# Optimization experiments

Hardware: AMD Instinct MI355X
Metric: run time of the kernel (lower is better)

## Reference

```python
import jax, jax.numpy as jnp
import numpy as np

B, R, T, D = 16, 1024, 512, 1024
H = 1024  # hidden_dim

def setup_inputs() -> dict:
    key = jax.random.key(0)
    ks = jax.random.split(key, 8)
    s_in = 1.0 / np.sqrt(D)
    s_comb = 1.0 / np.sqrt(3 * D)
    return {
        "region_feats": jax.random.normal(ks[0], (B, R, D), jnp.float32),
        "query_embs": jax.random.normal(ks[1], (B, T, D), jnp.float32),
        "Wr": jax.random.normal(ks[2], (D, H), jnp.float32) * s_in,
        "br": jnp.zeros((H,), jnp.float32),
        "Wq": jax.random.normal(ks[3], (D, H), jnp.float32) * s_in,
        "bq": jnp.zeros((H,), jnp.float32),
        "Ws": jax.random.normal(ks[4], (3 * D, 1), jnp.float32) * s_comb,
        "bs": jnp.zeros((1,), jnp.float32),
    }

def reference(region_feats, query_embs, Wr, br, Wq, bq, Ws, bs):
    # Dense projections
    R_proj = region_feats @ Wr + br            # [B,R,H]
    Q_proj = query_embs @ Wq + bq              # [B,T,H]
    # Unscaled cross-attention scores
    scores = jnp.einsum('brd,btd->brt', R_proj, Q_proj)  # [B,R,T]
    attn = jax.nn.softmax(scores, axis=-1)
    # Attend over RAW query embeddings (as in source)
    attended = jnp.einsum('brt,btd->brd', attn, query_embs)  # [B,R,D]
    combined = jnp.concatenate(
        [region_feats, attended, region_feats * attended], axis=-1)  # [B,R,3D]
    out = combined @ Ws + bs                    # [B,R,1]
    return jnp.squeeze(out, axis=-1)            # [B,R]
```

## Files before the change

### kernel.cpp

```cpp
#include <hip/hip_runtime.h>


#define BD 16
#define RD 1024
#define TD 512
#define DD 1024
#define BR (BD * RD)

typedef _Float16 half8 __attribute__((ext_vector_type(8)));
typedef _Float16 half4 __attribute__((ext_vector_type(4)));
typedef float floatx4 __attribute__((ext_vector_type(4)));

__device__ __forceinline__ float wave_sum(float v) {
#pragma unroll
  for (int off = 32; off > 0; off >>= 1) v += __shfl_down(v, off);
  return v;
}

__device__ __forceinline__ half8 cvt8(float4 a, float4 b) {
  half8 h = {(_Float16)a.x, (_Float16)a.y, (_Float16)a.z, (_Float16)a.w,
             (_Float16)b.x, (_Float16)b.y, (_Float16)b.z, (_Float16)b.w};
  return h;
}

__global__ __launch_bounds__(256) void prep_all(
    const float* __restrict__ Wr, const float* __restrict__ Wq,
    const float* __restrict__ Ws, const float* __restrict__ br,
    const float* __restrict__ region, const float* __restrict__ query,
    _Float16* __restrict__ M2, _Float16* __restrict__ Ws16,
    float* __restrict__ wqbr, _Float16* __restrict__ wqbr16,
    _Float16* __restrict__ r16, float* __restrict__ rdvec,
    _Float16* __restrict__ q16) {
  __shared__ __align__(16) _Float16 lds[2 * 2 * 2048];
  __shared__ float sm[4];
  const int blk = blockIdx.x, tid = threadIdx.x;

  if (blk < 256) {
    const int m0 = (blk >> 4) * 64, n0 = (blk & 15) * 64;
    const int lane = tid & 63, w = tid >> 6;
    const int wr = w >> 1, wc = w & 1;
    const int srow = tid >> 2, slot = tid & 3;
    const int scol = (slot ^ ((srow >> 1) & 3)) * 8;
    const long offA = (long)(m0 + srow) * DD + scol;
    const long offB = (long)(n0 + srow) * DD + scol;
    const int wofs = srow * 32 + slot * 8;
    const int NK = DD / 32;
    float4 a0, a1, b0, b1;
    a0 = *(const float4*)(Wr + offA); a1 = *(const float4*)(Wr + offA + 4);
    b0 = *(const float4*)(Wq + offB); b1 = *(const float4*)(Wq + offB + 4);
    *(int4*)&lds[wofs] = *(int4*)&(const half8&)cvt8(a0, a1);
    {
      half8 hb = cvt8(b0, b1);
      *(half8*)&lds[2048 + wofs] = hb;
    }
    a0 = *(const float4*)(Wr + offA + 32); a1 = *(const float4*)(Wr + offA + 36);
    b0 = *(const float4*)(Wq + offB + 32); b1 = *(const float4*)(Wq + offB + 36);
    __syncthreads();
    floatx4 acc[2][2] = {};
    const int fr = lane & 15, g = lane >> 4;
    const int fs = (g ^ ((fr >> 1) & 3)) * 8;
    for (int kt = 0; kt < NK; ++kt) {
      const int cur = (kt & 1) * 4096, nxt = ((kt + 1) & 1) * 4096;
      if (kt + 1 < NK) {
        half8 ha = cvt8(a0, a1), hb = cvt8(b0, b1);
        *(half8*)&lds[nxt + wofs] = ha;
        *(half8*)&lds[nxt + 2048 + wofs] = hb;
      }
      if (kt + 2 < NK) {
        const long go = (long)(kt + 2) * 32;
        a0 = *(const float4*)(Wr + offA + go); a1 = *(const float4*)(Wr + offA + go + 4);
        b0 = *(const float4*)(Wq + offB + go); b1 = *(const float4*)(Wq + offB + go + 4);
      }
      half8 af[2], bf[2];
#pragma unroll
      for (int i = 0; i < 2; ++i)
        af[i] = *(const half8*)&lds[cur + (32 * wr + 16 * i + fr) * 32 + fs];
#pragma unroll
      for (int j = 0; j < 2; ++j)
        bf[j] = *(const half8*)&lds[cur + 2048 + (32 * wc + 16 * j + fr) * 32 + fs];
#pragma unroll
      for (int i = 0; i < 2; ++i)
#pragma unroll
        for (int j = 0; j < 2; ++j)
          acc[i][j] = __builtin_amdgcn_mfma_f32_16x16x32_f16(af[i], bf[j], acc[i][j], 0, 0, 0);
      __syncthreads();
    }
    const int cr = g * 4, cc = fr;
#pragma unroll
    for (int i = 0; i < 2; ++i)
#pragma unroll
      for (int r = 0; r < 4; ++r)
#pragma unroll
        for (int j = 0; j < 2; ++j)
          M2[(long)(m0 + 32 * wr + 16 * i + cr + r) * DD + n0 + 32 * wc + 16 * j + cc] =
              (_Float16)acc[i][j][r];
  } else if (blk < 258) {
    const long i = (long)(blk - 256) * 1024 + tid * 4;
    const float4 v = *(const float4*)&Ws[DD + i];
    half4 h = {(_Float16)v.x, (_Float16)v.y, (_Float16)v.z, (_Float16)v.w};
    *(half4*)&Ws16[i] = h;
  } else if (blk < 514) {
    const int row = (blk - 258) * 4 + (tid >> 6);
    const int lane = tid & 63;
    const float* x = Wq + (long)row * DD;
    float s = 0.f;
    for (int k = lane; k < DD; k += 64) s += x[k] * br[k];
    s = wave_sum(s);
    if (lane == 0) {
      wqbr[row] = s;
      wqbr16[row] = (_Float16)s;
    }
  } else if (blk < 514 + BR) {
    const long row = blk - 514;
    const int lane = tid & 63, wid = tid >> 6;
    const long i = row * DD + tid * 4;
    const float4 v = *(const float4*)&region[i];
    half4 h = {(_Float16)v.x, (_Float16)v.y, (_Float16)v.z, (_Float16)v.w};
    *(half4*)&r16[i] = h;
    const float4 w0 = *(const float4*)&Ws[tid * 4];
    float rd = v.x * w0.x + v.y * w0.y + v.z * w0.z + v.w * w0.w;
    rd = wave_sum(rd);
    if (lane == 0) sm[wid] = rd;
    __syncthreads();
    if (tid == 0) rdvec[row] = sm[0] + sm[1] + sm[2] + sm[3];
  } else {
    const long row = blk - (514 + BR);
    const long i = row * DD + tid * 4;
    const float4 v = *(const float4*)&query[i];
    half4 h = {(_Float16)v.x, (_Float16)v.y, (_Float16)v.z, (_Float16)v.w};
    *(half4*)&q16[i] = h;
  }
}

__global__ __launch_bounds__(512, 4) void qp_gemm(
    const _Float16* __restrict__ A, const _Float16* __restrict__ B,
    _Float16* __restrict__ C, const _Float16* __restrict__ wq16,
    float* __restrict__ cvec) {
  __shared__ __align__(16) _Float16 lds[2 * 2 * 4096];
  const int lin = blockIdx.x;
  const int s = lin & 7, u = lin >> 3;
  const int mt = s * 8 + (u >> 3), nt = u & 7;
  const int m0 = mt * 128, n0 = nt * 128;
  const int tid = threadIdx.x, lane = tid & 63, w = tid >> 6;
  const int wr = w >> 1, wc = w & 1;

  const int lrow = lane >> 2, slot = lane & 3;
  const int scol = (slot ^ ((lrow >> 1) & 3)) * 8;
  const int srow = 16 * w + lrow;
  const _Float16* gA = A + (long)(m0 + srow) * DD + scol;
  const _Float16* gB = B + (long)(n0 + srow) * DD + scol;
  const int wofs = srow * 32 + slot * 8;

  const int NK = DD / 32;
  float cvp = 0.f;
  int4 pA, pB;
  pA = *(const int4*)gA;
  pB = *(const int4*)gB;
  {
    half8 qa, wb;
    __builtin_memcpy(&qa, &pA, 16);
    wb = *(const half8*)&wq16[scol];
#pragma unroll
    for (int e = 0; e < 8; ++e) cvp += (float)qa[e] * (float)wb[e];
  }
  *(int4*)&lds[wofs] = pA;
  *(int4*)&lds[4096 + wofs] = pB;
  pA = *(const int4*)(gA + 32);
  pB = *(const int4*)(gB + 32);
  __syncthreads();

  floatx4 acc[2][4] = {};
  const int fr = lane & 15, g = lane >> 4;
  const int fs = (g ^ ((fr >> 1) & 3)) * 8;

  for (int kt = 0; kt < NK; ++kt) {
    const int cur = (kt & 1) * 8192, nxt = ((kt + 1) & 1) * 8192;
    if (kt + 1 < NK) {
      half8 qa, wb;
      __builtin_memcpy(&qa, &pA, 16);
      wb = *(const half8*)&wq16[(kt + 1) * 32 + scol];
#pragma unroll
      for (int e = 0; e < 8; ++e) cvp += (float)qa[e] * (float)wb[e];
      *(int4*)&lds[nxt + wofs] = pA;
      *(int4*)&lds[nxt + 4096 + wofs] = pB;
    }
    if (kt + 2 < NK) {
      const long go = (long)(kt + 2) * 32;
      pA = *(const int4*)(gA + go);
      pB = *(const int4*)(gB + go);
    }
    half8 af[2], bf[4];
#pragma unroll
    for (int i = 0; i < 2; ++i)
      af[i] = *(const half8*)&lds[cur + (32 * wr + 16 * i + fr) * 32 + fs];
#pragma unroll
    for (int j = 0; j < 4; ++j)
      bf[j] = *(const half8*)&lds[cur + 4096 + (64 * wc + 16 * j + fr) * 32 + fs];
#pragma unroll
    for (int i = 0; i < 2; ++i)
#pragma unroll
      for (int j = 0; j < 4; ++j)
        acc[i][j] = __builtin_amdgcn_mfma_f32_16x16x32_f16(af[i], bf[j], acc[i][j], 0, 0, 0);
    __syncthreads();
  }

  cvp += __shfl_xor(cvp, 1);
  cvp += __shfl_xor(cvp, 2);
  if (nt == 0 && slot == 0) cvec[m0 + srow] = cvp;

  const int cr = g * 4, cc = fr;
#pragma unroll
  for (int i = 0; i < 2; ++i)
#pragma unroll
    for (int r = 0; r < 4; ++r)
#pragma unroll
      for (int j = 0; j < 4; ++j)
        C[(long)(m0 + 32 * wr + 16 * i + cr + r) * DD + n0 + 64 * wc + 16 * j + cc] =
            (_Float16)acc[i][j][r];
}

__global__ __launch_bounds__(512, 4) void gemm_fused(
    const _Float16* __restrict__ A, const _Float16* __restrict__ B0,
    const _Float16* __restrict__ B1,
    float* __restrict__ Ms, float* __restrict__ Ls, float* __restrict__ Hs,
    const float* __restrict__ cvec, const _Float16* __restrict__ wsh,
    long sA, long sB) {
  __shared__ __align__(16) _Float16 lds[2 * 3 * 4096];
  __shared__ __align__(16) _Float16 wlds[2048];

  const int lin = blockIdx.x;
  const int s = lin & 7, u = lin >> 3;
  const int b = 2 * s + (u >> 5);
  const int t = u & 31;
  const int mt = t >> 2, nt = t & 3;
  const int m0 = mt * 128, n0 = nt * 128;
  A += (long)b * sA;
  B0 += (long)b * sB;
  B1 += (long)b * sB;

  const int tid = threadIdx.x, lane = tid & 63, w = tid >> 6;
  const int wr = w >> 2, wc = w & 3;

  const int lrow = lane >> 2, slot = lane & 3;
  const int scol = (slot ^ ((lrow >> 1) & 3)) * 8;
  const int srow = 16 * w + lrow;
  const _Float16* gA = A + (long)(m0 + srow) * DD + scol;
  const _Float16* gP = B0 + (long)(n0 + srow) * DD + scol;
  const _Float16* gQ = B1 + (long)(n0 + srow) * DD + scol;
  const int wofs = srow * 32 + slot * 8;

  if (tid < 256) *(int4*)&wlds[tid * 8] = *(const int4*)&wsh[tid * 8];

  const int NK = DD / 32;
  int4 pA, pP, pQ;
  pA = *(const int4*)gA;
  pP = *(const int4*)gP;
  pQ = *(const int4*)gQ;
  *(int4*)&lds[wofs] = pA;
  *(int4*)&lds[4096 + wofs] = pP;
  *(int4*)&lds[8192 + wofs] = pQ;
  pA = *(const int4*)(gA + 32);
  pP = *(const int4*)(gP + 32);
  pQ = *(const int4*)(gQ + 32);
  __syncthreads();

  floatx4 accS[4][2] = {};
  floatx4 accH[4][2] = {};
  const int fr = lane & 15, g = lane >> 4;
  const int fs = (g ^ ((fr >> 1) & 3)) * 8;

  for (int kt = 0; kt < NK; ++kt) {
    const int cur = (kt & 1) * 12288;
    const int nxt = ((kt + 1) & 1) * 12288;
    if (kt + 1 < NK) {
      *(int4*)&lds[nxt + wofs] = pA;
      *(int4*)&lds[nxt + 4096 + wofs] = pP;
      *(int4*)&lds[nxt + 8192 + wofs] = pQ;
    }
    if (kt + 2 < NK) {
      const long go = (long)(kt + 2) * 32;
      pA = *(const int4*)(gA + go);
      pP = *(const int4*)(gP + go);
      pQ = *(const int4*)(gQ + go);
    }
    half8 af[4], bp[2], bq[2], w1f, w2f;
#pragma unroll
    for (int i = 0; i < 4; ++i)
      af[i] = *(const half8*)&lds[cur + (64 * wr + 16 * i + fr) * 32 + fs];
#pragma unroll
    for (int j = 0; j < 2; ++j)
      bp[j] = *(const half8*)&lds[cur + 4096 + (32 * wc + 16 * j + fr) * 32 + fs];
#pragma unroll
    for (int j = 0; j < 2; ++j)
      bq[j] = *(const half8*)&lds[cur + 8192 + (32 * wc + 16 * j + fr) * 32 + fs];
    w1f = *(const half8*)&wlds[kt * 32 + g * 8];
    w2f = *(const half8*)&wlds[1024 + kt * 32 + g * 8];
#pragma unroll
    for (int i = 0; i < 4; ++i)
#pragma unroll
      for (int j = 0; j < 2; ++j)
        accS[i][j] = __builtin_amdgcn_mfma_f32_16x16x32_f16(af[i], bp[j], accS[i][j], 0, 0, 0);
#pragma unroll
    for (int i = 0; i < 4; ++i) af[i] = w1f + af[i] * w2f;
#pragma unroll
    for (int i = 0; i < 4; ++i)
#pragma unroll
      for (int j = 0; j < 2; ++j)
        accH[i][j] = __builtin_amdgcn_mfma_f32_16x16x32_f16(af[i], bq[j], accH[i][j], 0, 0, 0);
    __syncthreads();
  }

  const int cr = g * 4, cc = fr;
  float cv[2];
#pragma unroll
  for (int j = 0; j < 2; ++j)
    cv[j] = cvec[(long)b * TD + n0 + 32 * wc + 16 * j + cc];
  const int chunk = nt * 4 + wc;
  const long rowBase = (long)b * RD + m0 + 64 * wr + cr;
#pragma unroll
  for (int i = 0; i < 4; ++i) {
#pragma unroll
    for (int r = 0; r < 4; ++r) {
      float mx = fmaxf(accS[i][0][r] + cv[0], accS[i][1][r] + cv[1]);
      mx = fmaxf(mx, __shfl_xor(mx, 1));
      mx = fmaxf(mx, __shfl_xor(mx, 2));
      mx = fmaxf(mx, __shfl_xor(mx, 4));
      mx = fmaxf(mx, __shfl_xor(mx, 8));
      float l = 0.f, hs = 0.f;
#pragma unroll
      for (int j = 0; j < 2; ++j) {
        const float e = __expf(accS[i][j][r] + cv[j] - mx);
        l += e;
        hs += e * accH[i][j][r];
      }
      l += __shfl_xor(l, 1); hs += __shfl_xor(hs, 1);
      l += __shfl_xor(l, 2); hs += __shfl_xor(hs, 2);
      l += __shfl_xor(l, 4); hs += __shfl_xor(hs, 4);
      l += __shfl_xor(l, 8); hs += __shfl_xor(hs, 8);
      if (cc == 0) {
        const long idx = (long)chunk * BR + rowBase + 16 * i + r;
        Ms[idx] = mx;
        Ls[idx] = l;
        Hs[idx] = hs;
      }
    }
  }
}

__global__ __launch_bounds__(256) void combine(
    const float* __restrict__ Ms, const float* __restrict__ Ls,
    const float* __restrict__ Hs, const float* __restrict__ rdvec,
    const float* __restrict__ bs, float* __restrict__ out) {
  const int row = blockIdx.x * 256 + threadIdx.x;
  float mv[16];
  float gm = -1e30f;
#pragma unroll
  for (int c = 0; c < 16; ++c) {
    mv[c] = Ms[(long)c * BR + row];
    gm = fmaxf(gm, mv[c]);
  }
  float L = 0.f, HS = 0.f;
#pragma unroll
  for (int c = 0; c < 16; ++c) {
    const float sc = __expf(mv[c] - gm);
    L += Ls[(long)c * BR + row] * sc;
    HS += Hs[(long)c * BR + row] * sc;
  }
  out[row] = HS / L + rdvec[row] + bs[0];
}

extern "C" void kernel_launch(void* const* d_in, const int* in_sizes, int n_in,
                              void* d_out, int out_size, void* d_ws, size_t ws_size,
                              hipStream_t stream) {
  const float* region = (const float*)d_in[0];
  const float* query  = (const float*)d_in[1];
  const float* Wr     = (const float*)d_in[2];
  const float* br     = (const float*)d_in[3];
  const float* Wq     = (const float*)d_in[4];
  const float* Ws     = (const float*)d_in[6];
  const float* bs     = (const float*)d_in[7];
  float* out = (float*)d_out;

  char* p = (char*)d_ws;
  _Float16* region16 = (_Float16*)p;
  _Float16* query16  = (_Float16*)(p + (32u << 20));
  _Float16* Qp       = (_Float16*)(p + (48u << 20));
  _Float16* M2       = (_Float16*)(p + (64u << 20));
  _Float16* Ws16     = (_Float16*)(p + (66u << 20));
  float*    wqbr     = (float*)(p + (66u << 20) + 8192);
  _Float16* wqbr16   = (_Float16*)(p + (66u << 20) + 12288);
  float*    cvec     = (float*)(p + (66u << 20) + 16384);
  float*    rdvec    = (float*)(p + (66u << 20) + 65536);
  float*    Ms       = (float*)(p + (67u << 20));
  float*    Ls       = Ms + 16 * BR;
  float*    Hs       = Ls + 16 * BR;

  prep_all<<<dim3(514 + BR + BD * TD), 256, 0, stream>>>(
      Wr, Wq, Ws, br, region, query, M2, Ws16, wqbr, wqbr16,
      region16, rdvec, query16);
  qp_gemm<<<dim3(512), 512, 0, stream>>>(query16, M2, Qp, wqbr16, cvec);
  gemm_fused<<<dim3(512), 512, 0, stream>>>(
      region16, Qp, query16, Ms, Ls, Hs, cvec, Ws16,
      (long)RD * DD, (long)TD * DD);
  combine<<<dim3(BR / 256), 256, 0, stream>>>(Ms, Ls, Hs, rdvec, bs, out);
}
```

Baseline: 219.5 us.

## Use direct global-to-LDS loads and fold Ws1 term into query-side vector

Both GEMM kernels now stage tiles with global_load_lds, copying straight into shared memory instead of going through registers and ds_write. This removes register staging and the two-deep prefetch. The attended·Ws1 term is factored algebraically: h1 = query·Ws1 is computed per query row in prep_all and added in the epilogue, and the per-k elementwise transform moves from the A fragments to the fewer B fragments (bq *= w2). The cvec dot product now reads the LDS fragments instead of the staged registers. Risks: prefetch depth drops to one tile, the LDS layout must line up with the swizzled reads, and fp16 rounding changes.

```diff
diff --git a/kernel.cpp b/kernel.cpp
--- a/kernel.cpp
+++ b/kernel.cpp
@@ -21,6 +21,12 @@
   half8 h = {(_Float16)a.x, (_Float16)a.y, (_Float16)a.z, (_Float16)a.w,
              (_Float16)b.x, (_Float16)b.y, (_Float16)b.z, (_Float16)b.w};
   return h;
+}
+
+__device__ __forceinline__ void gl16(const _Float16* g, _Float16* l) {
+  __builtin_amdgcn_global_load_lds(
+      (const __attribute__((address_space(1))) void*)g,
+      (__attribute__((address_space(3))) void*)l, 16, 0, 0);
 }
 
 __global__ __launch_bounds__(256) void prep_all(
@@ -30,7 +36,7 @@
     _Float16* __restrict__ M2, _Float16* __restrict__ Ws16,
     float* __restrict__ wqbr, _Float16* __restrict__ wqbr16,
     _Float16* __restrict__ r16, float* __restrict__ rdvec,
-    _Float16* __restrict__ q16) {
+    _Float16* __restrict__ q16, float* __restrict__ h1) {
   __shared__ __align__(16) _Float16 lds[2 * 2 * 2048];
   __shared__ float sm[4];
   const int blk = blockIdx.x, tid = threadIdx.x;
@@ -125,10 +131,17 @@
     if (tid == 0) rdvec[row] = sm[0] + sm[1] + sm[2] + sm[3];
   } else {
     const long row = blk - (514 + BR);
+    const int lane = tid & 63, wid = tid >> 6;
     const long i = row * DD + tid * 4;
     const float4 v = *(const float4*)&query[i];
     half4 h = {(_Float16)v.x, (_Float16)v.y, (_Float16)v.z, (_Float16)v.w};
     *(half4*)&q16[i] = h;
+    const float4 w1 = *(const float4*)&Ws[DD + tid * 4];
+    float hq = v.x * w1.x + v.y * w1.y + v.z * w1.z + v.w * w1.w;
+    hq = wave_sum(hq);
+    if (lane == 0) sm[wid] = hq;
+    __syncthreads();
+    if (tid == 0) h1[row] = sm[0] + sm[1] + sm[2] + sm[3];
   }
 }
 
@@ -149,45 +162,24 @@
   const int srow = 16 * w + lrow;
   const _Float16* gA = A + (long)(m0 + srow) * DD + scol;
   const _Float16* gB = B + (long)(n0 + srow) * DD + scol;
-  const int wofs = srow * 32 + slot * 8;
-
-  const int NK = DD / 32;
-  float cvp = 0.f;
-  int4 pA, pB;
-  pA = *(const int4*)gA;
-  pB = *(const int4*)gB;
-  {
-    half8 qa, wb;
-    __builtin_memcpy(&qa, &pA, 16);
-    wb = *(const half8*)&wq16[scol];
-#pragma unroll
-    for (int e = 0; e < 8; ++e) cvp += (float)qa[e] * (float)wb[e];
-  }
-  *(int4*)&lds[wofs] = pA;
-  *(int4*)&lds[4096 + wofs] = pB;
-  pA = *(const int4*)(gA + 32);
-  pB = *(const int4*)(gB + 32);
+  const int wbase = 512 * w;
+
+  gl16(gA, &lds[wbase]);
+  gl16(gB, &lds[4096 + wbase]);
   __syncthreads();
 
   floatx4 acc[2][4] = {};
+  float cvp[2] = {0.f, 0.f};
   const int fr = lane & 15, g = lane >> 4;
   const int fs = (g ^ ((fr >> 1) & 3)) * 8;
+  const int NK = DD / 32;
 
   for (int kt = 0; kt < NK; ++kt) {
-    const int cur = (kt & 1) * 8192, nxt = ((kt + 1) & 1) * 8192;
+    const int cur = (kt & 1) * 8192, nxt = cur ^ 8192;
     if (kt + 1 < NK) {
-      half8 qa, wb;
-      __builtin_memcpy(&qa, &pA, 16);
-      wb = *(const half8*)&wq16[(kt + 1) * 32 + scol];
-#pragma unroll
-      for (int e = 0; e < 8; ++e) cvp += (float)qa[e] * (float)wb[e];
-      *(int4*)&lds[nxt + wofs] = pA;
-      *(int4*)&lds[nxt + 4096 + wofs] = pB;
-    }
-    if (kt + 2 < NK) {
-      const long go = (long)(kt + 2) * 32;
-      pA = *(const int4*)(gA + go);
-      pB = *(const int4*)(gB + go);
+      const long go = (long)(kt + 1) * 32;
+      gl16(gA + go, &lds[nxt + wbase]);
+      gl16(gB + go, &lds[nxt + 4096 + wbase]);
     }
     half8 af[2], bf[4];
 #pragma unroll
@@ -196,6 +188,14 @@
 #pragma unroll
     for (int j = 0; j < 4; ++j)
       bf[j] = *(const half8*)&lds[cur + 4096 + (64 * wc + 16 * j + fr) * 32 + fs];
+    if (wc == 0) {
+      const half8 wb = *(const half8*)&wq16[kt * 32 + g * 8];
+#pragma unroll
+      for (int i = 0; i < 2; ++i)
+#pragma unroll
+        for (int e = 0; e < 8; ++e)
+          cvp[i] += (float)af[i][e] * (float)wb[e];
+    }
 #pragma unroll
     for (int i = 0; i < 2; ++i)
 #pragma unroll
@@ -204,9 +204,15 @@
     __syncthreads();
   }
 
-  cvp += __shfl_xor(cvp, 1);
-  cvp += __shfl_xor(cvp, 2);
-  if (nt == 0 && slot == 0) cvec[m0 + srow] = cvp;
+  if (wc == 0 && nt == 0) {
+#pragma unroll
+    for (int i = 0; i < 2; ++i) {
+      float c = cvp[i];
+      c += __shfl_xor(c, 16);
+      c += __shfl_xor(c, 32);
+      if (lane < 16) cvec[m0 + 32 * wr + 16 * i + lane] = c;
+    }
+  }
 
   const int cr = g * 4, cc = fr;
 #pragma unroll
@@ -223,10 +229,10 @@
     const _Float16* __restrict__ A, const _Float16* __restrict__ B0,
     const _Float16* __restrict__ B1,
     float* __restrict__ Ms, float* __restrict__ Ls, float* __restrict__ Hs,
-    const float* __restrict__ cvec, const _Float16* __restrict__ wsh,
-    long sA, long sB) {
+    const float* __restrict__ cvec, const float* __restrict__ h1,
+    const _Float16* __restrict__ wsh, long sA, long sB) {
   __shared__ __align__(16) _Float16 lds[2 * 3 * 4096];
-  __shared__ __align__(16) _Float16 wlds[2048];
+  __shared__ __align__(16) _Float16 wlds[1024];
 
   const int lin = blockIdx.x;
   const int s = lin & 7, u = lin >> 3;
@@ -247,43 +253,31 @@
   const _Float16* gA = A + (long)(m0 + srow) * DD + scol;
   const _Float16* gP = B0 + (long)(n0 + srow) * DD + scol;
   const _Float16* gQ = B1 + (long)(n0 + srow) * DD + scol;
-  const int wofs = srow * 32 + slot * 8;
-
-  if (tid < 256) *(int4*)&wlds[tid * 8] = *(const int4*)&wsh[tid * 8];
-
-  const int NK = DD / 32;
-  int4 pA, pP, pQ;
-  pA = *(const int4*)gA;
-  pP = *(const int4*)gP;
-  pQ = *(const int4*)gQ;
-  *(int4*)&lds[wofs] = pA;
-  *(int4*)&lds[4096 + wofs] = pP;
-  *(int4*)&lds[8192 + wofs] = pQ;
-  pA = *(const int4*)(gA + 32);
-  pP = *(const int4*)(gP + 32);
-  pQ = *(const int4*)(gQ + 32);
+  const int wbase = 512 * w;
+
+  if (tid < 128) *(int4*)&wlds[tid * 8] = *(const int4*)&wsh[1024 + tid * 8];
+
+  gl16(gA, &lds[wbase]);
+  gl16(gP, &lds[4096 + wbase]);
+  gl16(gQ, &lds[8192 + wbase]);
   __syncthreads();
 
   floatx4 accS[4][2] = {};
   floatx4 accH[4][2] = {};
   const int fr = lane & 15, g = lane >> 4;
   const int fs = (g ^ ((fr >> 1) & 3)) * 8;
+  const int NK = DD / 32;
 
   for (int kt = 0; kt < NK; ++kt) {
     const int cur = (kt & 1) * 12288;
-    const int nxt = ((kt + 1) & 1) * 12288;
+    const int nxt = cur ^ 12288;
     if (kt + 1 < NK) {
-      *(int4*)&lds[nxt + wofs] = pA;
-      *(int4*)&lds[nxt + 4096 + wofs] = pP;
-      *(int4*)&lds[nxt + 8192 + wofs] = pQ;
-    }
-    if (kt + 2 < NK) {
-      const long go = (long)(kt + 2) * 32;
-      pA = *(const int4*)(gA + go);
-      pP = *(const int4*)(gP + go);
-      pQ = *(const int4*)(gQ + go);
-    }
-    half8 af[4], bp[2], bq[2], w1f, w2f;
+      const long go = (long)(kt + 1) * 32;
+      gl16(gA + go, &lds[nxt + wbase]);
+      gl16(gP + go, &lds[nxt + 4096 + wbase]);
+      gl16(gQ + go, &lds[nxt + 8192 + wbase]);
+    }
+    half8 af[4], bp[2], bq[2];
 #pragma unroll
     for (int i = 0; i < 4; ++i)
       af[i] = *(const half8*)&lds[cur + (64 * wr + 16 * i + fr) * 32 + fs];
@@ -293,15 +287,14 @@
 #pragma unroll
     for (int j = 0; j < 2; ++j)
       bq[j] = *(const half8*)&lds[cur + 8192 + (32 * wc + 16 * j + fr) * 32 + fs];
-    w1f = *(const half8*)&wlds[kt * 32 + g * 8];
-    w2f = *(const half8*)&wlds[1024 + kt * 32 + g * 8];
+    const half8 w2f = *(const half8*)&wlds[kt * 32 + g * 8];
+#pragma unroll
+    for (int j = 0; j < 2; ++j) bq[j] *= w2f;
 #pragma unroll
     for (int i = 0; i < 4; ++i)
 #pragma unroll
       for (int j = 0; j < 2; ++j)
         accS[i][j] = __builtin_amdgcn_mfma_f32_16x16x32_f16(af[i], bp[j], accS[i][j], 0, 0, 0);
-#pragma unroll
-    for (int i = 0; i < 4; ++i) af[i] = w1f + af[i] * w2f;
 #pragma unroll
     for (int i = 0; i < 4; ++i)
 #pragma unroll
@@ -311,10 +304,13 @@
   }
 
   const int cr = g * 4, cc = fr;
-  float cv[2];
-#pragma unroll
-  for (int j = 0; j < 2; ++j)
-    cv[j] = cvec[(long)b * TD + n0 + 32 * wc + 16 * j + cc];
+  float cv[2], hv[2];
+#pragma unroll
+  for (int j = 0; j < 2; ++j) {
+    const long col = (long)b * TD + n0 + 32 * wc + 16 * j + cc;
+    cv[j] = cvec[col];
+    hv[j] = h1[col];
+  }
   const int chunk = nt * 4 + wc;
   const long rowBase = (long)b * RD + m0 + 64 * wr + cr;
 #pragma unroll
@@ -331,7 +327,7 @@
       for (int j = 0; j < 2; ++j) {
         const float e = __expf(accS[i][j][r] + cv[j] - mx);
         l += e;
-        hs += e * accH[i][j][r];
+        hs += e * (accH[i][j][r] + hv[j]);
       }
       l += __shfl_xor(l, 1); hs += __shfl_xor(hs, 1);
       l += __shfl_xor(l, 2); hs += __shfl_xor(hs, 2);
@@ -391,16 +387,17 @@
   _Float16* wqbr16   = (_Float16*)(p + (66u << 20) + 12288);
   float*    cvec     = (float*)(p + (66u << 20) + 16384);
   float*    rdvec    = (float*)(p + (66u << 20) + 65536);
+  float*    h1       = (float*)(p + (66u << 20) + 131072);
   float*    Ms       = (float*)(p + (67u << 20));
   float*    Ls       = Ms + 16 * BR;
   float*    Hs       = Ls + 16 * BR;
 
   prep_all<<<dim3(514 + BR + BD * TD), 256, 0, stream>>>(
       Wr, Wq, Ws, br, region, query, M2, Ws16, wqbr, wqbr16,
-      region16, rdvec, query16);
+      region16, rdvec, query16, h1);
   qp_gemm<<<dim3(512), 512, 0, stream>>>(query16, M2, Qp, wqbr16, cvec);
   gemm_fused<<<dim3(512), 512, 0, stream>>>(
-      region16, Qp, query16, Ms, Ls, Hs, cvec, Ws16,
+      region16, Qp, query16, Ms, Ls, Hs, cvec, h1, Ws16,
       (long)RD * DD, (long)TD * DD);
   combine<<<dim3(BR / 256), 256, 0, stream>>>(Ms, Ls, Hs, rdvec, bs, out);
 }
```

After: 218.0 us. Within noise of the previous version (-0.7%).
